# Kernel tuning notes

Hardware: AMD Instinct MI355X
Metric: run time of the kernel (lower is better)

## Reference

```python
import jax, jax.numpy as jnp
import numpy as np

M0, M1 = 32, 16          # multiplicities of 0e (scalars) and 1o (vectors)
FEAT = M0 + 3 * M1       # 80
WNUM = M0*M0 + M1*M1 + M0*M1 + M1*M0  # 2304 per-edge TP weights
N_NODES, N_EDGES, N_RBF, HID = 10000, 160000, 50, 64
EPS = 1e-5
INV_SQRT3 = 1.0 / np.sqrt(3.0)
# per-path normalization: 1/sqrt(num_paths_to_output * mul_in)
A_P1 = 1.0 / np.sqrt(2.0 * M0)   # 0e x 0e -> 0e
A_P4 = 1.0 / np.sqrt(2.0 * M1)   # 1o x 1o -> 0e
A_P2 = 1.0 / np.sqrt(2.0 * M1)   # 1o x 0e -> 1o
A_P3 = 1.0 / np.sqrt(2.0 * M0)   # 0e x 1o -> 1o


def setup_inputs() -> dict:
    key = jax.random.key(0)
    ks = jax.random.split(key, 12)
    def lin(k, fi, fo):
        return jax.random.normal(k, (fi, fo), jnp.float32) / np.sqrt(fi)
    return dict(
        h=jax.random.normal(ks[0], (N_NODES, FEAT), jnp.float32),
        edge_index=jax.random.randint(ks[1], (2, N_EDGES), 0, N_NODES),
        edge_sh=jax.random.normal(ks[2], (N_EDGES, 4), jnp.float32),
        edge_features=jax.random.normal(ks[3], (N_EDGES, N_RBF), jnp.float32),
        W1e=lin(ks[4], N_RBF, HID), b1e=jnp.zeros(HID, jnp.float32),
        W2e=lin(ks[5], HID, HID), b2e=jnp.zeros(HID, jnp.float32),
        W3e=lin(ks[6], HID, WNUM) * 0.1, b3e=jnp.zeros(WNUM, jnp.float32),
        A0=jax.random.normal(ks[7], (M0, M0), jnp.float32),
        A1p=jax.random.normal(ks[8], (M1, M1), jnp.float32),
        bn_w0=jnp.ones(M0, jnp.float32), bn_b0=jnp.zeros(M0, jnp.float32),
        bn_w1=jnp.ones(M1, jnp.float32),
    )


def _forward(h, edge_index, edge_sh, edge_features,
             W1e, b1e, W2e, b2e, W3e, b3e, A0, A1p, bn_w0, bn_b0, bn_w1):
    N = h.shape[0]
    E = edge_sh.shape[0]
    src, dst = edge_index[0], edge_index[1]

    # ---- edge MLP -> per-edge tensor-product weights [E, WNUM] ----
    w = jax.nn.silu(edge_features @ W1e + b1e)
    w = jax.nn.silu(w @ W2e + b2e)
    w = w @ W3e + b3e
    o1 = M0 * M0
    o2 = o1 + M1 * M1
    o3 = o2 + M0 * M1
    w1 = w[:, :o1].reshape(E, M0, M0)     # 0e x 0e -> 0e
    w2 = w[:, o1:o2].reshape(E, M1, M1)   # 1o x 0e -> 1o
    w3 = w[:, o2:o3].reshape(E, M0, M1)   # 0e x 1o -> 1o
    w4 = w[:, o3:].reshape(E, M1, M0)     # 1o x 1o -> 0e

    # ---- gather source node features ----
    s0 = h[src, :M0]                         # [E, M0]
    s1 = h[src, M0:].reshape(E, M1, 3)       # [E, M1, 3]
    y0 = edge_sh[:, 0]                       # [E]
    y1 = edge_sh[:, 1:4]                     # [E, 3]

    # ---- fully connected tensor product with per-edge weights ----
    # scalar output: 0e x 0e -> 0e  and  1o x 1o -> 0e (dot / sqrt(3))
    dot11 = jnp.einsum('eui,ei->eu', s1, y1) * INV_SQRT3      # [E, M1]
    m0 = (A_P1 * jnp.einsum('eu,euw->ew', s0 * y0[:, None], w1)
          + A_P4 * jnp.einsum('eu,euw->ew', dot11, w4))       # [E, M0]
    # vector output: 1o x 0e -> 1o  and  0e x 1o -> 1o
    m1 = (A_P2 * jnp.einsum('eui,euw->ewi', s1 * y0[:, None, None], w2)
          + A_P3 * jnp.einsum('eu,ei,euw->ewi', s0, y1, w3))  # [E, M1, 3]
    messages = jnp.concatenate([m0, m1.reshape(E, 3 * M1)], axis=1)  # [E, FEAT]

    # ---- scatter-mean aggregation to destination nodes ----
    agg = jax.ops.segment_sum(messages, dst, num_segments=N)
    cnt = jax.ops.segment_sum(jnp.ones((E,), messages.dtype), dst, num_segments=N)
    agg = agg / jnp.maximum(cnt, 1.0)[:, None]

    # ---- equivariant self-interaction (per-l linear mixing) ----
    self0 = (h[:, :M0] @ A0) / np.sqrt(M0)
    h1 = h[:, M0:].reshape(N, M1, 3)
    self1 = jnp.einsum('nui,uw->nwi', h1, A1p) / np.sqrt(M1)
    out = agg + jnp.concatenate([self0, self1.reshape(N, 3 * M1)], axis=1)

    # ---- equivariant batch norm (layer mode) ----
    x0 = out[:, :M0]
    x1 = out[:, M0:].reshape(N, M1, 3)
    mu = x0.mean(axis=0)
    var = x0.var(axis=0)
    x0n = (x0 - mu) * jax.lax.rsqrt(var + EPS) * bn_w0 + bn_b0
    nrm2 = (x1 ** 2).sum(axis=-1).mean(axis=0)               # [M1]
    x1n = x1 * (jax.lax.rsqrt(nrm2 + EPS) * bn_w1)[None, :, None]
    out = jnp.concatenate([x0n, x1n.reshape(N, 3 * M1)], axis=1)

    # ---- residual (irreps_in == irreps_out) ----
    return out + h


def reference(h, edge_index, edge_sh, edge_features,
              W1e, b1e, W2e, b2e, W3e, b3e, A0, A1p, bn_w0, bn_b0, bn_w1):
    return _forward(h, edge_index, edge_sh, edge_features,
                    W1e, b1e, W2e, b2e, W3e, b3e, A0, A1p, bn_w0, bn_b0, bn_w1)
```

## Files before the change

kernel.cpp:

```cpp
#include <hip/hip_runtime.h>
#include <math.h>

#define NN 10000
#define NE 160000
#define NRBF 50
#define WNUM 2304
#define EPSV 1e-5f

#define A_P1 0.125f
#define A_P2 0.17677669529663687f
#define A_P3 0.125f
#define A_P4 0.17677669529663687f
#define INV_SQRT3 0.5773502691896258f
#define INV_SQRT_M0 0.17677669529663687f
#define INV_SQRT_M1 0.25f

typedef __attribute__((ext_vector_type(8))) short bf16x8;
typedef __attribute__((ext_vector_type(4))) float f32x4;
typedef __attribute__((ext_vector_type(4))) int i32x4;

#define MFMA16(a, b, c) __builtin_amdgcn_mfma_f32_16x16x32_bf16(a, b, c, 0, 0, 0)

__device__ __forceinline__ short f2bf(float x) {
  unsigned u = __float_as_uint(x);
  unsigned r = (u + 0x7fffu + ((u >> 16) & 1u)) >> 16;
  return (short)r;
}

__global__ void prep_weights(const float* __restrict__ W1, const float* __restrict__ W2,
                             const float* __restrict__ W3, short* __restrict__ W1P,
                             short* __restrict__ W2P, short* __restrict__ W3P) {
  int s = blockIdx.x * 256 + threadIdx.x;
  if (s < WNUM * 64) {
    int t = s >> 10, r = s & 1023;
    int ch = r >> 9, l = (r >> 3) & 63, kk = r & 7;
    int row = t * 16 + (l & 15);
    int k = ((l >> 4) << 3) + (ch << 5) + kk;
    W3P[s] = f2bf(W3[k * WNUM + row]);
  } else if (s < WNUM * 64 + 4096) {
    int s2 = s - WNUM * 64;
    int t = s2 >> 10, r = s2 & 1023;
    int ch = r >> 9, l = (r >> 3) & 63, kk = r & 7;
    int row = t * 16 + (l & 15);
    int k = ((l >> 4) << 3) + (ch << 5) + kk;
    W1P[s2] = f2bf(k < NRBF ? W1[k * 64 + row] : 0.f);
  } else if (s < WNUM * 64 + 8192) {
    int s2 = s - WNUM * 64 - 4096;
    int t = s2 >> 10, r = s2 & 1023;
    int ch = r >> 9, l = (r >> 3) & 63, kk = r & 7;
    int row = t * 16 + (l & 15);
    int k = ((l >> 4) << 3) + (ch << 5) + kk;
    W2P[s2] = f2bf(W2[k * 64 + row]);
  }
}

__global__ __launch_bounds__(256, 3) void edge_kernel(
    const float* __restrict__ h, const int* __restrict__ eidx,
    const float* __restrict__ esh, const float* __restrict__ ef,
    const short* __restrict__ W1P, const float* __restrict__ b1,
    const short* __restrict__ W2P, const float* __restrict__ b2,
    const short* __restrict__ W3P, const float* __restrict__ b3,
    float* __restrict__ agg, float* __restrict__ cnt) {
  __shared__ short act[64 * 72];
  __shared__ float coef[6144];
  __shared__ float y0s[64], y1s[192];
  __shared__ float b1s[64], b2s[64];
  __shared__ int dsts[64];
  float* scratch = coef;

  const int tid = threadIdx.x;
  const int e0 = blockIdx.x * 64;

  for (int idx = tid; idx < 64 * 64; idx += 256) {
    int e = idx >> 6, k = idx & 63;
    float v = (k < NRBF) ? ef[(long)(e0 + e) * NRBF + k] : 0.f;
    act[e * 72 + k] = f2bf(v);
  }
  if (tid < 64) { b1s[tid] = b1[tid]; b2s[tid] = b2[tid]; }
  {
    int e = tid >> 2, q = tid & 3;
    int ge = e0 + e;
    int src = eidx[ge];
    float y0 = esh[ge * 4 + 0];
    float y1x = esh[ge * 4 + 1], y1y = esh[ge * 4 + 2], y1z = esh[ge * 4 + 3];
    const float* hs = h + (long)src * 80;
    for (int u = q; u < 32; u += 4) coef[u * 64 + e] = 0.125f * hs[u];
    for (int u = q; u < 16; u += 4) {
      float sx = hs[32 + u * 3], sy = hs[33 + u * 3], sz = hs[34 + u * 3];
      coef[2048 + u * 64 + e] = A_P2 * sx;
      coef[3072 + u * 64 + e] = A_P2 * sy;
      coef[4096 + u * 64 + e] = A_P2 * sz;
      coef[5120 + u * 64 + e] = A_P4 * INV_SQRT3 * (sx * y1x + sy * y1y + sz * y1z);
    }
    if (q == 0) {
      y0s[e] = y0;
      y1s[e] = y1x; y1s[64 + e] = y1y; y1s[128 + e] = y1z;
      dsts[e] = eidx[NE + ge];
    }
  }
  __syncthreads();

  const int wid = tid >> 6, l = tid & 63;
  const int lr = l & 15, lg = l >> 4;
  const int g16 = lg * 4;
  const int er = wid * 16;

  {
    bf16x8 a0 = *(const bf16x8*)&act[(er + lr) * 72 + lg * 8];
    bf16x8 a1 = *(const bf16x8*)&act[(er + lr) * 72 + 32 + lg * 8];
#pragma unroll
    for (int jt = 0; jt < 4; ++jt) {
      const short* wb = W1P + (jt << 10) + (l << 3);
      bf16x8 b0 = *(const bf16x8*)wb;
      bf16x8 b1f = *(const bf16x8*)(wb + 512);
      float bias = b1s[jt * 16 + lr];
      f32x4 d = {bias, bias, bias, bias};
      d = MFMA16(a0, b0, d);
      d = MFMA16(a1, b1f, d);
#pragma unroll
      for (int r = 0; r < 4; ++r) {
        float x = d[r];
        x = x / (1.f + __expf(-x));
        act[(er + lg * 4 + r) * 72 + jt * 16 + lr] = f2bf(x);
      }
    }
  }
  {
    bf16x8 a0 = *(const bf16x8*)&act[(er + lr) * 72 + lg * 8];
    bf16x8 a1 = *(const bf16x8*)&act[(er + lr) * 72 + 32 + lg * 8];
#pragma unroll
    for (int jt = 0; jt < 4; ++jt) {
      const short* wb = W2P + (jt << 10) + (l << 3);
      bf16x8 b0 = *(const bf16x8*)wb;
      bf16x8 b1f = *(const bf16x8*)(wb + 512);
      float bias = b2s[jt * 16 + lr];
      f32x4 d = {bias, bias, bias, bias};
      d = MFMA16(a0, b0, d);
      d = MFMA16(a1, b1f, d);
#pragma unroll
      for (int r = 0; r < 4; ++r) {
        float x = d[r];
        x = x / (1.f + __expf(-x));
        act[(er + lg * 4 + r) * 72 + jt * 16 + lr] = f2bf(x);
      }
    }
  }
  __syncthreads();

  bf16x8 a0g[4], a1g[4];
#pragma unroll
  for (int g = 0; g < 4; ++g) {
    a0g[g] = *(const bf16x8*)&act[(g * 16 + lr) * 72 + lg * 8];
    a1g[g] = *(const bf16x8*)&act[(g * 16 + lr) * 72 + 32 + lg * 8];
  }

#define M0_PAIR(TE, COFF)                                            \
  {                                                                  \
    const short* wbE = W3P + ((TE) << 10) + (l << 3);                \
    const short* wbO = W3P + (((TE) + 1) << 10) + (l << 3);          \
    bf16x8 E0 = *(const bf16x8*)wbE;                                 \
    bf16x8 E1 = *(const bf16x8*)(wbE + 512);                         \
    bf16x8 O0 = *(const bf16x8*)wbO;                                 \
    bf16x8 O1 = *(const bf16x8*)(wbO + 512);                         \
    float be = b3[((TE) << 4) + lr];                                 \
    float bo = b3[(((TE) + 1) << 4) + lr];                           \
    _Pragma("unroll")                                                \
    for (int g = 0; g < 4; ++g) {                                    \
      f32x4 c = *(const f32x4*)&coef[(COFF) + g * 16 + g16];         \
      f32x4 d = {be, be, be, be};                                    \
      d = MFMA16(a0g[g], E0, d);                                     \
      f32x4 v = MFMA16(a1g[g], E1, d);                               \
      f32x4 d2 = {bo, bo, bo, bo};                                   \
      d2 = MFMA16(a0g[g], O0, d2);                                   \
      f32x4 v2 = MFMA16(a1g[g], O1, d2);                             \
      _Pragma("unroll")                                              \
      for (int r = 0; r < 4; ++r) {                                  \
        acc0[g][r] += c[r] * v[r];                                   \
        acc1[g][r] += c[r] * v2[r];                                  \
      }                                                              \
    }                                                                \
  }

#define W2_TILE(U)                                                   \
  {                                                                  \
    const short* wb = W3P + ((64 + (U)) << 10) + (l << 3);           \
    bf16x8 B0 = *(const bf16x8*)wb;                                  \
    bf16x8 B1 = *(const bf16x8*)(wb + 512);                          \
    float bb = b3[((64 + (U)) << 4) + lr];                           \
    _Pragma("unroll")                                                \
    for (int g = 0; g < 4; ++g) {                                    \
      f32x4 d = {bb, bb, bb, bb};                                    \
      d = MFMA16(a0g[g], B0, d);                                     \
      f32x4 v = MFMA16(a1g[g], B1, d);                               \
      f32x4 cx = *(const f32x4*)&coef[2048 + (U) * 64 + g * 16 + g16]; \
      f32x4 cy = *(const f32x4*)&coef[3072 + (U) * 64 + g * 16 + g16]; \
      f32x4 cz = *(const f32x4*)&coef[4096 + (U) * 64 + g * 16 + g16]; \
      _Pragma("unroll")                                              \
      for (int r = 0; r < 4; ++r) {                                  \
        mx[g][r] += cx[r] * v[r];                                    \
        my[g][r] += cy[r] * v[r];                                    \
        mz[g][r] += cz[r] * v[r];                                    \
      }                                                              \
    }                                                                \
  }

#define W3_TILE(U)                                                   \
  {                                                                  \
    const short* wb = W3P + ((80 + (U)) << 10) + (l << 3);           \
    bf16x8 B0 = *(const bf16x8*)wb;                                  \
    bf16x8 B1 = *(const bf16x8*)(wb + 512);                          \
    float bb = b3[((80 + (U)) << 4) + lr];                           \
    _Pragma("unroll")                                                \
    for (int g = 0; g < 4; ++g) {                                    \
      f32x4 d = {bb, bb, bb, bb};                                    \
      d = MFMA16(a0g[g], B0, d);                                     \
      f32x4 v = MFMA16(a1g[g], B1, d);                               \
      f32x4 c = *(const f32x4*)&coef[(U) * 64 + g * 16 + g16];       \
      _Pragma("unroll")                                              \
      for (int r = 0; r < 4; ++r) t3[g][r] += c[r] * v[r];           \
    }                                                                \
  }

  if (wid < 2) {
    f32x4 acc0[4], acc1[4];
#pragma unroll
    for (int g = 0; g < 4; ++g) {
      acc0[g] = (f32x4){0, 0, 0, 0};
      acc1[g] = (f32x4){0, 0, 0, 0};
    }
    if (wid == 0) {
#pragma unroll 2
      for (int u = 0; u < 24; ++u) M0_PAIR(2 * u, u * 64);
#pragma unroll
      for (int g = 0; g < 4; ++g) {
        f32x4 y0v = *(const f32x4*)&y0s[g * 16 + g16];
#pragma unroll
        for (int r = 0; r < 4; ++r) { acc0[g][r] *= y0v[r]; acc1[g][r] *= y0v[r]; }
      }
    } else {
#pragma unroll 2
      for (int u = 24; u < 32; ++u) M0_PAIR(2 * u, u * 64);
#pragma unroll
      for (int g = 0; g < 4; ++g) {
        f32x4 y0v = *(const f32x4*)&y0s[g * 16 + g16];
#pragma unroll
        for (int r = 0; r < 4; ++r) { acc0[g][r] *= y0v[r]; acc1[g][r] *= y0v[r]; }
      }
#pragma unroll 2
      for (int p = 0; p < 16; ++p) M0_PAIR(112 + 2 * p, 5120 + p * 64);
    }
    __syncthreads();
    if (wid == 1) {
      float* p = scratch + l * 20;
      *(f32x4*)(p + 0) = acc0[0]; *(f32x4*)(p + 4) = acc1[0];
      *(f32x4*)(p + 8) = acc0[1]; *(f32x4*)(p + 12) = acc1[1];
    } else {
      float* p = scratch + 1280 + l * 20;
      *(f32x4*)(p + 0) = acc0[2]; *(f32x4*)(p + 4) = acc1[2];
      *(f32x4*)(p + 8) = acc0[3]; *(f32x4*)(p + 12) = acc1[3];
    }
    __syncthreads();
    const int gb = (wid == 0) ? 0 : 2;
    const float* p = (wid == 0) ? (scratch + l * 20) : (scratch + 1280 + l * 20);
    f32x4 t0 = *(const f32x4*)(p + 0), t1 = *(const f32x4*)(p + 4);
    f32x4 t2 = *(const f32x4*)(p + 8), t3_ = *(const f32x4*)(p + 12);
    i32x4 dd0 = *(const i32x4*)&dsts[(gb + 0) * 16 + g16];
    i32x4 dd1 = *(const i32x4*)&dsts[(gb + 1) * 16 + g16];
#pragma unroll
    for (int r = 0; r < 4; ++r) {
      float* base = agg + (long)dd0[r] * 80;
      atomicAdd(base + lr, acc0[gb + 0][r] + t0[r]);
      atomicAdd(base + 16 + lr, acc1[gb + 0][r] + t1[r]);
    }
#pragma unroll
    for (int r = 0; r < 4; ++r) {
      float* base = agg + (long)dd1[r] * 80;
      atomicAdd(base + lr, acc0[gb + 1][r] + t2[r]);
      atomicAdd(base + 16 + lr, acc1[gb + 1][r] + t3_[r]);
    }
  } else {
    f32x4 mx[4], my[4], mz[4], t3[4];
#pragma unroll
    for (int g = 0; g < 4; ++g) {
      mx[g] = (f32x4){0, 0, 0, 0}; my[g] = (f32x4){0, 0, 0, 0};
      mz[g] = (f32x4){0, 0, 0, 0}; t3[g] = (f32x4){0, 0, 0, 0};
    }
    if (wid == 2) {
#pragma unroll 2
      for (int u = 0; u < 8; ++u) W2_TILE(u);
#pragma unroll 2
      for (int u = 0; u < 16; ++u) W3_TILE(u);
    } else {
#pragma unroll 2
      for (int u = 8; u < 16; ++u) W2_TILE(u);
#pragma unroll 2
      for (int u = 16; u < 32; ++u) W3_TILE(u);
    }
#pragma unroll
    for (int g = 0; g < 4; ++g) {
      f32x4 y0v = *(const f32x4*)&y0s[g * 16 + g16];
      f32x4 yx = *(const f32x4*)&y1s[g * 16 + g16];
      f32x4 yy = *(const f32x4*)&y1s[64 + g * 16 + g16];
      f32x4 yz = *(const f32x4*)&y1s[128 + g * 16 + g16];
#pragma unroll
      for (int r = 0; r < 4; ++r) {
        mx[g][r] = mx[g][r] * y0v[r] + yx[r] * t3[g][r];
        my[g][r] = my[g][r] * y0v[r] + yy[r] * t3[g][r];
        mz[g][r] = mz[g][r] * y0v[r] + yz[r] * t3[g][r];
      }
    }
    __syncthreads();
    if (wid == 3) {
      float* p = scratch + 2560 + l * 28;
      *(f32x4*)(p + 0) = mx[0]; *(f32x4*)(p + 4) = my[0]; *(f32x4*)(p + 8) = mz[0];
      *(f32x4*)(p + 12) = mx[1]; *(f32x4*)(p + 16) = my[1]; *(f32x4*)(p + 20) = mz[1];
    } else {
      float* p = scratch + 4352 + l * 28;
      *(f32x4*)(p + 0) = mx[2]; *(f32x4*)(p + 4) = my[2]; *(f32x4*)(p + 8) = mz[2];
      *(f32x4*)(p + 12) = mx[3]; *(f32x4*)(p + 16) = my[3]; *(f32x4*)(p + 20) = mz[3];
    }
    __syncthreads();
    const int gb = (wid == 2) ? 0 : 2;
    const float* p = (wid == 2) ? (scratch + 2560 + l * 28) : (scratch + 4352 + l * 28);
    f32x4 u0 = *(const f32x4*)(p + 0), u1 = *(const f32x4*)(p + 4);
    f32x4 u2 = *(const f32x4*)(p + 8), u3 = *(const f32x4*)(p + 12);
    f32x4 u4 = *(const f32x4*)(p + 16), u5 = *(const f32x4*)(p + 20);
    i32x4 dd0 = *(const i32x4*)&dsts[(gb + 0) * 16 + g16];
    i32x4 dd1 = *(const i32x4*)&dsts[(gb + 1) * 16 + g16];
#pragma unroll
    for (int r = 0; r < 4; ++r) {
      float* base = agg + (long)dd0[r] * 80;
      atomicAdd(base + 32 + lr * 3 + 0, mx[gb + 0][r] + u0[r]);
      atomicAdd(base + 32 + lr * 3 + 1, my[gb + 0][r] + u1[r]);
      atomicAdd(base + 32 + lr * 3 + 2, mz[gb + 0][r] + u2[r]);
    }
#pragma unroll
    for (int r = 0; r < 4; ++r) {
      float* base = agg + (long)dd1[r] * 80;
      atomicAdd(base + 32 + lr * 3 + 0, mx[gb + 1][r] + u3[r]);
      atomicAdd(base + 32 + lr * 3 + 1, my[gb + 1][r] + u4[r]);
      atomicAdd(base + 32 + lr * 3 + 2, mz[gb + 1][r] + u5[r]);
    }
  }
  if (tid < 64) atomicAdd(cnt + dsts[tid], 1.0f);
#undef M0_PAIR
#undef W2_TILE
#undef W3_TILE
}

__global__ __launch_bounds__(256) void node_a(
    const float* __restrict__ h, const float* __restrict__ A0,
    const float* __restrict__ A1p, const float* __restrict__ agg,
    const float* __restrict__ cnt, float* __restrict__ outpre,
    float* __restrict__ stats) {
  __shared__ float redw[4][80];
  const int tid = threadIdx.x;
  const int wid = tid >> 6, l = tid & 63;
  const int n = blockIdx.x * 256 + tid;
  float x0[32], x1[48];
#pragma unroll
  for (int w = 0; w < 32; w++) x0[w] = 0.f;
#pragma unroll
  for (int c = 0; c < 48; c++) x1[c] = 0.f;
  if (n < NN) {
    const float* hr = h + (long)n * 80;
    const float* ar = agg + (long)n * 80;
    float inv = 1.f / fmaxf(cnt[n], 1.f);
#pragma unroll 1
    for (int u = 0; u < 32; u++) {
      float hu = hr[u];
#pragma unroll
      for (int w = 0; w < 32; w++) x0[w] += hu * A0[u * 32 + w];
    }
#pragma unroll
    for (int w = 0; w < 32; w++) x0[w] = x0[w] * INV_SQRT_M0 + ar[w] * inv;
#pragma unroll 1
    for (int u = 0; u < 16; u++) {
      float a = hr[32 + u * 3], b_ = hr[33 + u * 3], c_ = hr[34 + u * 3];
#pragma unroll
      for (int w = 0; w < 16; w++) {
        float Aw = A1p[u * 16 + w];
        x1[w * 3 + 0] += a * Aw;
        x1[w * 3 + 1] += b_ * Aw;
        x1[w * 3 + 2] += c_ * Aw;
      }
    }
#pragma unroll
    for (int c = 0; c < 48; c++) x1[c] = x1[c] * INV_SQRT_M1 + ar[32 + c] * inv;
    float* opr = outpre + (long)n * 80;
#pragma unroll
    for (int w = 0; w < 32; w++) opr[w] = x0[w];
#pragma unroll
    for (int c = 0; c < 48; c++) opr[32 + c] = x1[c];
  }
#pragma unroll 1
  for (int c = 0; c < 32; ++c) {
    float s = x0[c];
#pragma unroll
    for (int m = 32; m >= 1; m >>= 1) s += __shfl_xor(s, m, 64);
    if (l == 0) redw[wid][c] = s;
  }
#pragma unroll 1
  for (int c = 0; c < 32; ++c) {
    float v = x0[c];
    float s = v * v;
#pragma unroll
    for (int m = 32; m >= 1; m >>= 1) s += __shfl_xor(s, m, 64);
    if (l == 0) redw[wid][32 + c] = s;
  }
#pragma unroll 1
  for (int u = 0; u < 16; ++u) {
    float s = x1[u * 3] * x1[u * 3] + x1[u * 3 + 1] * x1[u * 3 + 1] +
              x1[u * 3 + 2] * x1[u * 3 + 2];
#pragma unroll
    for (int m = 32; m >= 1; m >>= 1) s += __shfl_xor(s, m, 64);
    if (l == 0) redw[wid][64 + u] = s;
  }
  __syncthreads();
  if (tid < 80)
    atomicAdd(&stats[tid],
              redw[0][tid] + redw[1][tid] + redw[2][tid] + redw[3][tid]);
}

__global__ void node_b(const float* __restrict__ outpre, const float* __restrict__ stats,
                       const float* __restrict__ bnw0, const float* __restrict__ bnb0,
                       const float* __restrict__ bnw1, const float* __restrict__ h,
                       float* __restrict__ out) {
  int idx = blockIdx.x * 256 + threadIdx.x;
  if (idx >= NN * 80) return;
  int c = idx % 80;
  float v = outpre[idx];
  const float invN = 1.f / NN;
  float o;
  if (c < 32) {
    float mu = stats[c] * invN;
    float var = stats[32 + c] * invN - mu * mu;
    o = (v - mu) * rsqrtf(var + EPSV) * bnw0[c] + bnb0[c];
  } else {
    int u = (c - 32) / 3;
    float nr = stats[64 + u] * invN;
    o = v * rsqrtf(nr + EPSV) * bnw1[u];
  }
  out[idx] = o + h[idx];
}

extern "C" void kernel_launch(void* const* d_in, const int* in_sizes, int n_in,
                              void* d_out, int out_size, void* d_ws, size_t ws_size,
                              hipStream_t stream) {
  const float* h    = (const float*)d_in[0];
  const int*   eidx = (const int*)d_in[1];
  const float* esh  = (const float*)d_in[2];
  const float* ef   = (const float*)d_in[3];
  const float* W1   = (const float*)d_in[4];
  const float* b1   = (const float*)d_in[5];
  const float* W2   = (const float*)d_in[6];
  const float* b2   = (const float*)d_in[7];
  const float* W3   = (const float*)d_in[8];
  const float* b3   = (const float*)d_in[9];
  const float* A0   = (const float*)d_in[10];
  const float* A1p  = (const float*)d_in[11];
  const float* bnw0 = (const float*)d_in[12];
  const float* bnb0 = (const float*)d_in[13];
  const float* bnw1 = (const float*)d_in[14];
  float* out = (float*)d_out;

  float* ws = (float*)d_ws;
  float* agg    = ws;
  float* cnt    = ws + 800000;
  float* stats  = ws + 810000;
  float* outpre = ws + 810080;
  short* W3P    = (short*)(ws + 1610080);
  short* W1P    = W3P + WNUM * 64;
  short* W2P    = W1P + 4096;

  hipMemsetAsync(agg, 0, (size_t)810080 * sizeof(float), stream);

  prep_weights<<<(WNUM * 64 + 8192 + 255) / 256, 256, 0, stream>>>(W1, W2, W3, W1P,
                                                                   W2P, W3P);
  edge_kernel<<<NE / 64, 256, 0, stream>>>(h, eidx, esh, ef, W1P, b1, W2P, b2, W3P, b3,
                                           agg, cnt);
  node_a<<<(NN + 255) / 256, 256, 0, stream>>>(h, A0, A1p, agg, cnt, outpre, stats);
  node_b<<<(NN * 80 + 255) / 256, 256, 0, stream>>>(outpre, stats, bnw0, bnb0, bnw1, h,
                                                    out);
}
```

Measured before the change: 227.9 us.

## Parallelize node_a across output channels with one wave per node

node_a used to run one thread per node, with 80 accumulators per thread and only 40 blocks in the grid. It now gives each node to a wavefront, where each lane computes one or two output channels, and stages A0 and A1p in shared memory. The grid grows to 625 blocks. BN statistics are reduced with shared-memory atomics instead of shuffle trees. The goal is better occupancy and coalesced loads and stores, at the cost of contended LDS atomics. Node_a is small next to the edge kernel, so the effect on total time is limited.

Measured after the change: 204.2 us (median of 2 runs). 10.4% less time.

```diff
diff --git a/kernel.cpp b/kernel.cpp
--- a/kernel.cpp
+++ b/kernel.cpp
@@ -353,73 +353,66 @@
     const float* __restrict__ A1p, const float* __restrict__ agg,
     const float* __restrict__ cnt, float* __restrict__ outpre,
     float* __restrict__ stats) {
-  __shared__ float redw[4][80];
+  __shared__ float A0s[1024], A1ps[256], red[80];
   const int tid = threadIdx.x;
+  for (int i = tid; i < 1280; i += 256) {
+    if (i < 1024) A0s[i] = A0[i];
+    else A1ps[i - 1024] = A1p[i - 1024];
+  }
+  if (tid < 80) red[tid] = 0.f;
+  __syncthreads();
   const int wid = tid >> 6, l = tid & 63;
-  const int n = blockIdx.x * 256 + tid;
-  float x0[32], x1[48];
-#pragma unroll
-  for (int w = 0; w < 32; w++) x0[w] = 0.f;
-#pragma unroll
-  for (int c = 0; c < 48; c++) x1[c] = 0.f;
-  if (n < NN) {
+
+  float s1 = 0.f, s2 = 0.f, s3 = 0.f;
+
+  const int jA = l - 32;
+  const int wA = (l >= 32) ? jA / 3 : 0;
+  const int iA = (l >= 32) ? jA - wA * 3 : 0;
+  const int jB = 32 + l;
+  const int wB = jB / 3;
+  const int iB = jB - wB * 3;
+
+#pragma unroll 1
+  for (int it = 0; it < 4; ++it) {
+    const int n = blockIdx.x * 16 + wid * 4 + it;
     const float* hr = h + (long)n * 80;
     const float* ar = agg + (long)n * 80;
-    float inv = 1.f / fmaxf(cnt[n], 1.f);
-#pragma unroll 1
-    for (int u = 0; u < 32; u++) {
-      float hu = hr[u];
-#pragma unroll
-      for (int w = 0; w < 32; w++) x0[w] += hu * A0[u * 32 + w];
-    }
-#pragma unroll
-    for (int w = 0; w < 32; w++) x0[w] = x0[w] * INV_SQRT_M0 + ar[w] * inv;
-#pragma unroll 1
-    for (int u = 0; u < 16; u++) {
-      float a = hr[32 + u * 3], b_ = hr[33 + u * 3], c_ = hr[34 + u * 3];
-#pragma unroll
-      for (int w = 0; w < 16; w++) {
-        float Aw = A1p[u * 16 + w];
-        x1[w * 3 + 0] += a * Aw;
-        x1[w * 3 + 1] += b_ * Aw;
-        x1[w * 3 + 2] += c_ * Aw;
-      }
-    }
-#pragma unroll
-    for (int c = 0; c < 48; c++) x1[c] = x1[c] * INV_SQRT_M1 + ar[32 + c] * inv;
-    float* opr = outpre + (long)n * 80;
-#pragma unroll
-    for (int w = 0; w < 32; w++) opr[w] = x0[w];
-#pragma unroll
-    for (int c = 0; c < 48; c++) opr[32 + c] = x1[c];
-  }
-#pragma unroll 1
-  for (int c = 0; c < 32; ++c) {
-    float s = x0[c];
-#pragma unroll
-    for (int m = 32; m >= 1; m >>= 1) s += __shfl_xor(s, m, 64);
-    if (l == 0) redw[wid][c] = s;
-  }
-#pragma unroll 1
-  for (int c = 0; c < 32; ++c) {
-    float v = x0[c];
-    float s = v * v;
-#pragma unroll
-    for (int m = 32; m >= 1; m >>= 1) s += __shfl_xor(s, m, 64);
-    if (l == 0) redw[wid][32 + c] = s;
-  }
-#pragma unroll 1
-  for (int u = 0; u < 16; ++u) {
-    float s = x1[u * 3] * x1[u * 3] + x1[u * 3 + 1] * x1[u * 3 + 1] +
-              x1[u * 3 + 2] * x1[u * 3 + 2];
-#pragma unroll
-    for (int m = 32; m >= 1; m >>= 1) s += __shfl_xor(s, m, 64);
-    if (l == 0) redw[wid][64 + u] = s;
-  }
+    const float inv = 1.f / fmaxf(cnt[n], 1.f);
+    float valA;
+    if (l < 32) {
+      float x = 0.f;
+#pragma unroll 8
+      for (int u = 0; u < 32; ++u) x += hr[u] * A0s[u * 32 + l];
+      valA = x * INV_SQRT_M0 + ar[l] * inv;
+    } else {
+      float x = 0.f;
+#pragma unroll 8
+      for (int u = 0; u < 16; ++u) x += hr[32 + u * 3 + iA] * A1ps[u * 16 + wA];
+      valA = x * INV_SQRT_M1 + ar[l] * inv;
+    }
+    float valB = 0.f;
+    if (l < 16) {
+      float x = 0.f;
+#pragma unroll 8
+      for (int u = 0; u < 16; ++u) x += hr[32 + u * 3 + iB] * A1ps[u * 16 + wB];
+      valB = x * INV_SQRT_M1 + ar[64 + l] * inv;
+    }
+    outpre[(long)n * 80 + l] = valA;
+    if (l < 16) outpre[(long)n * 80 + 64 + l] = valB;
+    if (l < 32) { s1 += valA; s2 += valA * valA; }
+    else s2 += valA * valA;
+    if (l < 16) s3 += valB * valB;
+  }
+
+  if (l < 32) {
+    atomicAdd(&red[l], s1);
+    atomicAdd(&red[32 + l], s2);
+  } else {
+    atomicAdd(&red[64 + wA], s2);
+  }
+  if (l < 16) atomicAdd(&red[64 + wB], s3);
   __syncthreads();
-  if (tid < 80)
-    atomicAdd(&stats[tid],
-              redw[0][tid] + redw[1][tid] + redw[2][tid] + redw[3][tid]);
+  if (tid < 80) atomicAdd(&stats[tid], red[tid]);
 }
 
 __global__ void node_b(const float* __restrict__ outpre, const float* __restrict__ stats,
@@ -479,7 +472,7 @@
                                                                    W2P, W3P);
   edge_kernel<<<NE / 64, 256, 0, stream>>>(h, eidx, esh, ef, W1P, b1, W2P, b2, W3P, b3,
                                            agg, cnt);
-  node_a<<<(NN + 255) / 256, 256, 0, stream>>>(h, A0, A1p, agg, cnt, outpre, stats);
+  node_a<<<NN / 16, 256, 0, stream>>>(h, A0, A1p, agg, cnt, outpre, stats);
   node_b<<<(NN * 80 + 255) / 256, 256, 0, stream>>>(outpre, stats, bnw0, bnb0, bnw1, h,
                                                     out);
 }
```
